# Optimization experiments

Hardware: AMD Instinct MI355X
Metric: run time of the kernel (lower is better)

## Reference

```python
import jax, jax.numpy as jnp
import numpy as np

N_QUBITS = 14
N_LAYERS = 3
BATCH = 128


def _apply_1q(state, gate, w, n):
    """Apply a single-qubit gate on wire w (PennyLane wire 0 = most significant bit).
    state: (B, 2**n) complex. gate: (2,2) shared or (B,2,2) batched."""
    L, R = 2 ** w, 2 ** (n - 1 - w)
    s = state.reshape(-1, L, 2, R)
    if gate.ndim == 2:
        s = jnp.einsum('ij,aljr->alir', gate, s)
    else:
        s = jnp.einsum('aij,aljr->alir', gate, s)
    return s.reshape(state.shape)


def _apply_cnot(state, c, t, n):
    """CNOT with control wire c, target wire t on (B, 2**n) state."""
    s = state.reshape((-1,) + (2,) * n)
    ca = 1 + c
    s0 = jax.lax.index_in_dim(s, 0, ca, keepdims=False)
    s1 = jax.lax.index_in_dim(s, 1, ca, keepdims=False)
    # axis of target after removing control axis
    ta = 1 + t if t < c else t
    s1 = jnp.flip(s1, axis=ta)
    return jnp.stack([s0, s1], axis=ca).reshape(state.shape)


def _rx_gates(angles):
    """Batched RX gate matrices. angles: (B,) -> (B,2,2) complex64."""
    half = angles * 0.5
    c = jnp.cos(half).astype(jnp.complex64)
    s = (-1j) * jnp.sin(half).astype(jnp.complex64)
    return jnp.stack([jnp.stack([c, s], -1), jnp.stack([s, c], -1)], -2)


def _rot_gate(phi, theta, omega):
    """PennyLane Rot(phi,theta,omega) = RZ(omega) RY(theta) RZ(phi), (2,2) complex."""
    ct = jnp.cos(theta * 0.5).astype(jnp.complex64)
    st = jnp.sin(theta * 0.5).astype(jnp.complex64)
    ep = jnp.exp(-0.5j * (phi + omega))  # e^{-i(phi+omega)/2}
    em = jnp.exp(-0.5j * (phi - omega))  # e^{-i(phi-omega)/2}
    return jnp.stack([
        jnp.stack([ep * ct, -jnp.conj(em) * st]),
        jnp.stack([em * st, jnp.conj(ep) * ct]),
    ]).astype(jnp.complex64)


def _simulate(x, q_weights):
    B, n = x.shape
    state = jnp.zeros((B, 2 ** n), jnp.complex64).at[:, 0].set(1.0)
    # AngleEmbedding: RX(x_i) on wire i
    for w in range(n):
        state = _apply_1q(state, _rx_gates(x[:, w]), w, n)
    # StronglyEntanglingLayers: Rot on each wire, then ring of CNOTs with range r
    n_layers = q_weights.shape[0]
    for l in range(n_layers):
        for w in range(n):
            g = _rot_gate(q_weights[l, w, 0], q_weights[l, w, 1], q_weights[l, w, 2])
            state = _apply_1q(state, g, w, n)
        r = (l % (n - 1)) + 1  # PennyLane default ranges
        for w in range(n):
            state = _apply_cnot(state, w, (w + r) % n, n)
    return state


def _pauli_z_signs(n):
    idx = np.arange(2 ** n, dtype=np.int64)[:, None]
    shifts = np.arange(n - 1, -1, -1, dtype=np.int64)[None, :]  # wire 0 = MSB
    bits = (idx >> shifts) & 1
    return jnp.asarray(1.0 - 2.0 * bits, dtype=jnp.float32)  # (2**n, n)


def setup_inputs() -> dict:
    key = jax.random.key(0)
    k1, k2, k3, k4 = jax.random.split(key, 4)
    x = jax.random.normal(k1, (BATCH, N_QUBITS), dtype=jnp.float32)
    q_weights = jax.random.normal(k2, (N_LAYERS, N_QUBITS, 3), dtype=jnp.float32) * 0.01
    w_lin = jax.random.normal(k3, (1, N_QUBITS), dtype=jnp.float32) / np.sqrt(N_QUBITS)
    b_lin = jax.random.normal(k4, (1,), dtype=jnp.float32) * 0.01
    return {"x": x, "q_weights": q_weights, "w_lin": w_lin, "b_lin": b_lin}


def reference(x, q_weights, w_lin, b_lin):
    n = x.shape[1]
    state = _simulate(x, q_weights)
    probs = (state.real ** 2 + state.imag ** 2).astype(jnp.float32)  # (B, 2**n)
    expvals = probs @ _pauli_z_signs(n)  # (B, n) = <Z_i>
    logits = expvals @ w_lin.T + b_lin  # (B, 1)
    return logits
```

## Files before the change

kernel.cpp:

```cpp
#include <hip/hip_runtime.h>
#include <string.h>

#define NQ 14
#define NSTATE (1 << NQ)
#define NL 3
#define MAXP 12
#define BT 1024
#define NWAVES (BT / 64)

struct PassG {
    unsigned cmb8[16];
    unsigned R[10];
    unsigned gidx[4];
    unsigned nw;
    unsigned pad;
};
struct ParamsG {
    PassG pass[MAXP];
    unsigned ms[NQ];
    unsigned fmask[NQ];
};

struct C2x2 { float2 m[2][2]; };

__device__ __forceinline__ float2 cmul(float2 a, float2 b) {
    return make_float2(a.x * b.x - a.y * b.y, a.x * b.y + a.y * b.x);
}
__device__ __forceinline__ float2 cmac(float2 acc, float2 a, float2 b) {
    acc.x = fmaf(a.x, b.x, fmaf(-a.y, b.y, acc.x));
    acc.y = fmaf(a.x, b.y, fmaf(a.y, b.x, acc.y));
    return acc;
}

__device__ __forceinline__ C2x2 rot_gate(const float* qp) {
    float phi = qp[0], th = qp[1], om = qp[2];
    float ct, stt; __sincosf(0.5f * th, &stt, &ct);
    float sa, ca; __sincosf(0.5f * (phi + om), &sa, &ca);
    float sb, cb; __sincosf(0.5f * (phi - om), &sb, &cb);
    C2x2 G;
    G.m[0][0] = make_float2(ca * ct, -sa * ct);
    G.m[0][1] = make_float2(-cb * stt, -sb * stt);
    G.m[1][0] = make_float2(cb * stt, -sb * stt);
    G.m[1][1] = make_float2(ca * ct, sa * ct);
    return G;
}

__device__ __forceinline__ C2x2 fuse_rx(C2x2 G, float ang) {
    float sh, ch; __sincosf(0.5f * ang, &sh, &ch);
    float2 c = make_float2(ch, 0.f), is = make_float2(0.f, -sh);
    C2x2 R;
    #pragma unroll
    for (int i = 0; i < 2; ++i) {
        R.m[i][0] = cmac(cmul(G.m[i][0], c), G.m[i][1], is);
        R.m[i][1] = cmac(cmul(G.m[i][1], c), G.m[i][0], is);
    }
    return R;
}

__device__ __forceinline__ void load_pass(const PassG* __restrict__ p, int tid,
        unsigned cmb[16], unsigned gidx[4], unsigned& nw, unsigned& r)
{
    const uint4* c4 = (const uint4*)p->cmb8;
    uint4 u0 = c4[0], u1 = c4[1], u2 = c4[2], u3 = c4[3];
    cmb[0] = u0.x; cmb[1] = u0.y; cmb[2]  = u0.z; cmb[3]  = u0.w;
    cmb[4] = u1.x; cmb[5] = u1.y; cmb[6]  = u1.z; cmb[7]  = u1.w;
    cmb[8] = u2.x; cmb[9] = u2.y; cmb[10] = u2.z; cmb[11] = u2.w;
    cmb[12] = u3.x; cmb[13] = u3.y; cmb[14] = u3.z; cmb[15] = u3.w;
    unsigned rr = 0;
    #pragma unroll
    for (int j = 0; j < 10; ++j)
        rr ^= ((tid >> j) & 1) ? p->R[j] : 0u;
    r = rr;
    #pragma unroll
    for (int q = 0; q < 4; ++q) gidx[q] = p->gidx[q];
    nw = p->nw;
}

#define APPLY_STAGES()                                                      \
    {                                                                       \
        _Pragma("unroll")                                                   \
        for (int q = 0; q < 4; ++q) {                                       \
            if (q < (int)nwr) {                    \
                const int gi = (int)gidxr[q] * 4;                           \
                float2 g00 = gbuf[gi + 0], g01 = gbuf[gi + 1];              \
                float2 g10 = gbuf[gi + 2], g11 = gbuf[gi + 3];              \
                _Pragma("unroll")                                           \
                for (int i = 0; i < 16; ++i) {                              \
                    if (!((i >> q) & 1)) {                                  \
                        const int i1 = i | (1 << q);                        \
                        float2 a0 = a[i], a1 = a[i1];                       \
                        float2 n0 = cmac(cmul(g00, a0), g01, a1);           \
                        float2 n1 = cmac(cmul(g10, a0), g11, a1);           \
                        a[i] = n0; a[i1] = n1;                              \
                    }                                                       \
                }                                                           \
            }                                                               \
        }                                                                   \
    }

__global__ __launch_bounds__(BT) void qsim_kernel(
    const float* __restrict__ x, const float* __restrict__ qw,
    const float* __restrict__ wl, const float* __restrict__ bl,
    float* __restrict__ out, const ParamsG* __restrict__ pp, int np)
{
    __shared__ float2 st[NSTATE];
    __shared__ float2 gbuf[NL * NQ * 4];
    __shared__ float red[NWAVES];

    const int tid = threadIdx.x;
    const int b = blockIdx.x;

    if (tid < NL * NQ) {
        int l = tid / NQ, w = tid % NQ;
        C2x2 G = rot_gate(qw + tid * 3);
        if (l == 0) G = fuse_rx(G, x[b * NQ + w]);
        gbuf[tid * 4 + 0] = G.m[0][0];
        gbuf[tid * 4 + 1] = G.m[0][1];
        gbuf[tid * 4 + 2] = G.m[1][0];
        gbuf[tid * 4 + 3] = G.m[1][1];
    }

    char* sb = (char*)st;
    float2 a[16];
    unsigned addr[16];
    unsigned cmbreg[16], gidxr[4], nwr, rn;

    load_pass(&pp->pass[0], tid, cmbreg, gidxr, nwr, rn);

    __syncthreads();

    {
        const unsigned rb = rn << 3;
        #pragma unroll
        for (int i = 0; i < 16; ++i) addr[i] = rb ^ cmbreg[i];
        #pragma unroll
        for (int i = 0; i < 16; ++i) a[i] = make_float2(0.f, 0.f);
        if (tid == 0) {
            a[0] = make_float2(1.f, 0.f);
            APPLY_STAGES();
        }
        #pragma unroll
        for (int i = 0; i < 16; ++i)
            *(float2*)(sb + addr[i]) = a[i];
    }

    load_pass(&pp->pass[1], tid, cmbreg, gidxr, nwr, rn);

    #pragma unroll 1
    for (int ps = 1; ps < np - 1; ++ps) {
        __syncthreads();
        const unsigned rb = rn << 3;
        #pragma unroll
        for (int i = 0; i < 16; ++i) addr[i] = rb ^ cmbreg[i];
        #pragma unroll
        for (int i = 0; i < 16; ++i)
            a[i] = *(const float2*)(sb + addr[i]);
        unsigned cmbn[16], gidxn[4], nwn, rnn;
        load_pass(&pp->pass[ps + 1], tid, cmbn, gidxn, nwn, rnn);
        APPLY_STAGES();
        #pragma unroll
        for (int i = 0; i < 16; ++i)
            *(float2*)(sb + addr[i]) = a[i];
        #pragma unroll
        for (int i = 0; i < 16; ++i) cmbreg[i] = cmbn[i];
        #pragma unroll
        for (int q = 0; q < 4; ++q) gidxr[q] = gidxn[q];
        nwr = nwn; rn = rnn;
    }

    float acc = 0.f;
    {
        __syncthreads();
        const unsigned rb = rn << 3;
        #pragma unroll
        for (int i = 0; i < 16; ++i) addr[i] = rb ^ cmbreg[i];
        #pragma unroll
        for (int i = 0; i < 16; ++i)
            a[i] = *(const float2*)(sb + addr[i]);
        APPLY_STAGES();

        float A[16];
        #pragma unroll
        for (int i = 0; i < 16; ++i) A[i] = 0.f;
        #pragma unroll
        for (int w = 0; w < NQ; ++w) {
            float v = wl[w];
            unsigned p0 = __popc(rn & pp->ms[w]) & 1u;
            float vs = p0 ? -v : v;
            const unsigned fm = pp->fmask[w];
            #pragma unroll
            for (int i = 0; i < 16; ++i)
                A[i] += ((fm >> i) & 1u) ? -vs : vs;
        }
        #pragma unroll
        for (int i = 0; i < 16; ++i)
            acc = fmaf(fmaf(a[i].x, a[i].x, a[i].y * a[i].y), A[i], acc);
    }

    #pragma unroll
    for (int off = 32; off > 0; off >>= 1) acc += __shfl_down(acc, off, 64);
    if ((tid & 63) == 0) red[tid >> 6] = acc;
    __syncthreads();
    if (tid == 0) {
        float s2 = 0.f;
        #pragma unroll
        for (int i = 0; i < NWAVES; ++i) s2 += red[i];
        out[b] = s2 + bl[0];
    }
}

struct GF2Basis {
    unsigned piv[NQ];
    GF2Basis() { for (int i = 0; i < NQ; ++i) piv[i] = 0; }
    bool insert(unsigned v) {
        for (int bb = NQ - 1; bb >= 0; --bb) {
            if (!((v >> bb) & 1)) continue;
            if (piv[bb]) v ^= piv[bb];
            else { piv[bb] = v; return true; }
        }
        return false;
    }
};

static inline int par16(unsigned v) { return __builtin_parity(v); }
static inline unsigned lcg_next(unsigned& s) { s = s * 1664525u + 1013904223u; return s >> 8; }

static unsigned gf_apply(const unsigned* C, unsigned v) {
    unsigned r = 0;
    while (v) { int j = __builtin_ctz(v); v &= v - 1; r ^= C[j]; }
    return r;
}

static bool gf_invert(const unsigned* C, unsigned* Ci) {
    unsigned rows[NQ], irows[NQ];
    for (int i = 0; i < NQ; ++i) {
        unsigned r = 0;
        for (int j = 0; j < NQ; ++j) r |= ((C[j] >> i) & 1u) << j;
        rows[i] = r; irows[i] = 1u << i;
    }
    for (int c = 0; c < NQ; ++c) {
        int p = -1;
        for (int r = c; r < NQ; ++r) if ((rows[r] >> c) & 1u) { p = r; break; }
        if (p < 0) return false;
        unsigned t = rows[p]; rows[p] = rows[c]; rows[c] = t;
        t = irows[p]; irows[p] = irows[c]; irows[c] = t;
        for (int r = 0; r < NQ; ++r)
            if (r != c && ((rows[r] >> c) & 1u)) { rows[r] ^= rows[c]; irows[r] ^= irows[c]; }
    }
    for (int j = 0; j < NQ; ++j) {
        unsigned col = 0;
        for (int i = 0; i < NQ; ++i) col |= ((irows[i] >> j) & 1u) << i;
        Ci[j] = col;
    }
    return true;
}

extern "C" void kernel_launch(void* const* d_in, const int* in_sizes, int n_in,
                              void* d_out, int out_size, void* d_ws, size_t ws_size,
                              hipStream_t stream) {
    const float* x  = (const float*)d_in[0];
    const float* qw = (const float*)d_in[1];
    const float* wl = (const float*)d_in[2];
    const float* bl = (const float*)d_in[3];
    float* out = (float*)d_out;

    const int B = in_sizes[0] / NQ;

    unsigned gs[NL * NQ], gm[NL * NQ];
    int ggi[NL * NQ];
    unsigned s[NQ], m[NQ], msIdx[NQ];
    for (int w = 0; w < NQ; ++w) s[w] = m[w] = 1u << (NQ - 1 - w);
    int ng = 0;
    for (int l = 0; l < NL; ++l) {
        for (int w = 0; w < NQ; ++w) {
            gs[ng] = s[w]; gm[ng] = m[w]; ggi[ng] = l * NQ + w; ++ng;
        }
        int r = (l % (NQ - 1)) + 1;
        for (int w = 0; w < NQ; ++w) {
            int c = w, t = (w + r) % NQ;
            s[t] ^= s[c];
            m[c] ^= m[t];
        }
    }
    for (int w = 0; w < NQ; ++w) msIdx[w] = s[w];

    struct Raw { unsigned rv[10], cmb[16]; unsigned char gidx[4], nw; } raw[MAXP];
    bool used[NL * NQ] = {false};
    int np = 0, remaining = ng;
    while (remaining > 0 && np < MAXP) {
        unsigned pss[4], pmm[4];
        int pgi[4], nw = 0;
        GF2Basis gf;
        for (int g = 0; g < ng && nw < 4; ++g) {
            if (used[g]) continue;
            bool ok = true;
            for (int k = 0; k < nw && ok; ++k)
                if (par16(gs[g] & pmm[k]) || par16(pss[k] & gm[g])) ok = false;
            for (int h = 0; h < g && ok; ++h)
                if (!used[h] && (par16(gs[g] & gm[h]) || par16(gs[h] & gm[g]))) ok = false;
            if (!ok) continue;
            GF2Basis trial = gf;
            if (!trial.insert(gm[g])) continue;
            gf = trial;
            pss[nw] = gs[g]; pmm[nw] = gm[g]; pgi[nw] = g; ++nw;
            used[g] = true; --remaining;
        }
        unsigned mm[4], ss[4];
        for (int i = 0; i < nw; ++i) { mm[i] = pmm[i]; ss[i] = pss[i]; }
        for (int i = nw; i < 4; ++i) {
            unsigned cand = 0;
            for (int t = 0; t < NQ; ++t)
                if (gf.insert(1u << t)) { cand = 1u << t; break; }
            for (int j = 0; j < nw; ++j)
                if (par16(cand & ss[j])) cand ^= mm[j];
            mm[i] = cand; ss[i] = 0;
        }
        int nR = 0;
        for (int t = 0; t < NQ && nR < 10; ++t) {
            if (gf.insert(1u << t)) {
                unsigned v = 1u << t;
                for (int j = 0; j < nw; ++j)
                    if (par16(v & ss[j])) v ^= mm[j];
                raw[np].rv[nR++] = v;
            }
        }
        for (int idx = 0; idx < 16; ++idx) {
            unsigned c = 0;
            for (int q = 0; q < 4; ++q) if ((idx >> q) & 1) c ^= mm[q];
            raw[np].cmb[idx] = c;
        }
        for (int q = 0; q < 4; ++q)
            raw[np].gidx[q] = (unsigned char)(q < nw ? ggi[pgi[q]] : 0);
        raw[np].nw = (unsigned char)nw;
        ++np;
    }

    unsigned Cm[NQ], Ci[NQ];
    unsigned seed = 0x9E3779B9u;
    bool found = false;
    for (int tries = 0; tries < 5000 && !found; ++tries) {
        for (int j = 0; j < NQ; ++j) Cm[j] = lcg_next(seed) & (NSTATE - 1);
        if (!gf_invert(Cm, Ci)) continue;
        found = true;
        for (int p = 0; p < np && found; ++p) {
            unsigned piv[4] = {0, 0, 0, 0}; int npv = 0;
            for (int i = 0; i < 10; ++i) {
                unsigned w2 = gf_apply(Cm, raw[p].rv[i]);
                for (int bb = 0; bb < 4; ++bb)
                    if (((w2 >> bb) & 1u) && piv[bb]) w2 ^= piv[bb];
                if ((w2 & 15u) && npv < 4) { piv[__builtin_ctz(w2 & 15u)] = w2; ++npv; }
            }
            if (npv < 4) found = false;
        }
    }
    if (!found) {
        for (int j = 0; j < NQ; ++j) Cm[j] = 1u << j;
        gf_invert(Cm, Ci);
    }

    static ParamsG h_pg;
    memset(&h_pg, 0, sizeof(h_pg));
    for (int p = 0; p < np; ++p) {
        unsigned u[10];
        for (int i = 0; i < 10; ++i) u[i] = gf_apply(Cm, raw[p].rv[i]);
        unsigned piv[4] = {0, 0, 0, 0};
        int ord[10], npv = 0, rest[10], nrest = 0;
        for (int i = 0; i < 10; ++i) {
            unsigned w2 = u[i];
            for (int bb = 0; bb < 4; ++bb)
                if (((w2 >> bb) & 1u) && piv[bb]) w2 ^= piv[bb];
            if ((w2 & 15u) && npv < 4) { piv[__builtin_ctz(w2 & 15u)] = w2; ord[npv++] = i; }
            else rest[nrest++] = i;
        }
        int kk = 0;
        for (int i = 0; i < npv; ++i) h_pg.pass[p].R[kk++] = u[ord[i]];
        for (int i = 0; i < nrest; ++i) h_pg.pass[p].R[kk++] = u[rest[i]];
        for (int idx = 0; idx < 16; ++idx)
            h_pg.pass[p].cmb8[idx] = gf_apply(Cm, raw[p].cmb[idx]) << 3;
        for (int q = 0; q < 4; ++q) h_pg.pass[p].gidx[q] = raw[p].gidx[q];
        h_pg.pass[p].nw = raw[p].nw;
    }
    for (int w = 0; w < NQ; ++w) {
        unsigned msp = 0;
        for (int i = 0; i < NQ; ++i)
            msp |= (unsigned)(par16(Ci[i] & msIdx[w]) & 1) << i;
        h_pg.ms[w] = msp;
    }
    for (int w = 0; w < NQ; ++w) {
        unsigned fm = 0;
        for (int i = 0; i < 16; ++i)
            fm |= (unsigned)(par16((h_pg.pass[np - 1].cmb8[i] >> 3) & h_pg.ms[w]) & 1) << i;
        h_pg.fmask[w] = fm;
    }

    ParamsG* d_pg = (ParamsG*)d_ws;
    hipMemcpyAsync(d_pg, &h_pg, sizeof(ParamsG), hipMemcpyHostToDevice, stream);
    qsim_kernel<<<dim3(B), dim3(BT), 0, stream>>>(x, qw, wl, bl, out, d_pg, np);
}
```

Before: 109.6 us.

## Initialize state as product state analytically, drop layer-0 gate passes

Because the first layer (RX fused with Rot) acts on the |0> state before any CNOT, the result is a product state. Each thread now computes its 16 amplitudes directly as products of per-wire first-column gate entries. Layer-0 gates are no longer scheduled into the GF(2)-permuted pass plan, and pass 0 becomes a fixed identity-layout pass. This removes whole shared-memory gate passes in exchange for extra host-side index mapping (initIW) and a small per-thread product computation.

```diff
diff --git a/kernel.cpp b/kernel.cpp
--- a/kernel.cpp
+++ b/kernel.cpp
@@ -19,6 +19,7 @@
     PassG pass[MAXP];
     unsigned ms[NQ];
     unsigned fmask[NQ];
+    unsigned initIW[10];
 };
 
 struct C2x2 { float2 m[2][2]; };
@@ -105,6 +106,7 @@
 {
     __shared__ float2 st[NSTATE];
     __shared__ float2 gbuf[NL * NQ * 4];
+    __shared__ float2 ubuf[NQ][2];
     __shared__ float red[NWAVES];
 
     const int tid = threadIdx.x;
@@ -113,7 +115,11 @@
     if (tid < NL * NQ) {
         int l = tid / NQ, w = tid % NQ;
         C2x2 G = rot_gate(qw + tid * 3);
-        if (l == 0) G = fuse_rx(G, x[b * NQ + w]);
+        if (l == 0) {
+            G = fuse_rx(G, x[b * NQ + w]);
+            ubuf[w][0] = G.m[0][0];
+            ubuf[w][1] = G.m[1][0];
+        }
         gbuf[tid * 4 + 0] = G.m[0][0];
         gbuf[tid * 4 + 1] = G.m[0][1];
         gbuf[tid * 4 + 2] = G.m[1][0];
@@ -127,21 +133,39 @@
 
     load_pass(&pp->pass[0], tid, cmbreg, gidxr, nwr, rn);
 
+    unsigned b0 = 0;
+    #pragma unroll
+    for (int j = 0; j < 10; ++j)
+        b0 ^= ((tid >> j) & 1) ? pp->initIW[j] : 0u;
+
     __syncthreads();
 
     {
         const unsigned rb = rn << 3;
-        #pragma unroll
-        for (int i = 0; i < 16; ++i) addr[i] = rb ^ cmbreg[i];
-        #pragma unroll
-        for (int i = 0; i < 16; ++i) a[i] = make_float2(0.f, 0.f);
-        if (tid == 0) {
-            a[0] = make_float2(1.f, 0.f);
-            APPLY_STAGES();
-        }
-        #pragma unroll
-        for (int i = 0; i < 16; ++i)
-            *(float2*)(sb + addr[i]) = a[i];
+        float2 c = ubuf[0][b0 & 1];
+        #pragma unroll
+        for (int w = 1; w < 10; ++w)
+            c = cmul(c, ubuf[w][(b0 >> w) & 1]);
+        a[0] = cmul(c, ubuf[10][0]);
+        a[1] = cmul(c, ubuf[10][1]);
+        #pragma unroll
+        for (int i = 0; i < 2; ++i) {
+            a[2 + i] = cmul(a[i], ubuf[11][1]);
+            a[i]     = cmul(a[i], ubuf[11][0]);
+        }
+        #pragma unroll
+        for (int i = 0; i < 4; ++i) {
+            a[4 + i] = cmul(a[i], ubuf[12][1]);
+            a[i]     = cmul(a[i], ubuf[12][0]);
+        }
+        #pragma unroll
+        for (int i = 0; i < 8; ++i) {
+            a[8 + i] = cmul(a[i], ubuf[13][1]);
+            a[i]     = cmul(a[i], ubuf[13][0]);
+        }
+        #pragma unroll
+        for (int i = 0; i < 16; ++i)
+            *(float2*)(sb + (rb ^ cmbreg[i])) = a[i];
     }
 
     load_pass(&pp->pass[1], tid, cmbreg, gidxr, nwr, rn);
@@ -272,8 +296,10 @@
     for (int w = 0; w < NQ; ++w) s[w] = m[w] = 1u << (NQ - 1 - w);
     int ng = 0;
     for (int l = 0; l < NL; ++l) {
-        for (int w = 0; w < NQ; ++w) {
-            gs[ng] = s[w]; gm[ng] = m[w]; ggi[ng] = l * NQ + w; ++ng;
+        if (l > 0) {
+            for (int w = 0; w < NQ; ++w) {
+                gs[ng] = s[w]; gm[ng] = m[w]; ggi[ng] = l * NQ + w; ++ng;
+            }
         }
         int r = (l % (NQ - 1)) + 1;
         for (int w = 0; w < NQ; ++w) {
@@ -285,8 +311,22 @@
     for (int w = 0; w < NQ; ++w) msIdx[w] = s[w];
 
     struct Raw { unsigned rv[10], cmb[16]; unsigned char gidx[4], nw; } raw[MAXP];
+
+    {
+        unsigned mm[4];
+        for (int q = 0; q < 4; ++q) mm[q] = 1u << (3 - q);
+        for (int j = 0; j < 10; ++j) raw[0].rv[j] = 1u << (13 - j);
+        for (int idx = 0; idx < 16; ++idx) {
+            unsigned c = 0;
+            for (int q = 0; q < 4; ++q) if ((idx >> q) & 1) c ^= mm[q];
+            raw[0].cmb[idx] = c;
+        }
+        for (int q = 0; q < 4; ++q) raw[0].gidx[q] = 0;
+        raw[0].nw = 0;
+    }
+
     bool used[NL * NQ] = {false};
-    int np = 0, remaining = ng;
+    int np = 1, remaining = ng;
     while (remaining > 0 && np < MAXP) {
         unsigned pss[4], pmm[4];
         int pgi[4], nw = 0;
@@ -392,6 +432,21 @@
             fm |= (unsigned)(par16((h_pg.pass[np - 1].cmb8[i] >> 3) & h_pg.ms[w]) & 1) << i;
         h_pg.fmask[w] = fm;
     }
+    {
+        unsigned tmask[NQ];
+        for (int w = 0; w < NQ; ++w) {
+            unsigned t = 0;
+            for (int i = 0; i < NQ; ++i)
+                t |= (unsigned)((Ci[i] >> (NQ - 1 - w)) & 1u) << i;
+            tmask[w] = t;
+        }
+        for (int j = 0; j < 10; ++j) {
+            unsigned iw = 0;
+            for (int w = 0; w < NQ; ++w)
+                iw |= (unsigned)(par16(h_pg.pass[0].R[j] & tmask[w]) & 1) << w;
+            h_pg.initIW[j] = iw;
+        }
+    }
 
     ParamsG* d_pg = (ParamsG*)d_ws;
     hipMemcpyAsync(d_pg, &h_pg, sizeof(ParamsG), hipMemcpyHostToDevice, stream);
```

New measurement: 100.2 us. 8.6% less time.
